# Kernel optimization log

Measured on AMD Instinct MI355X. Metric: run time of the kernel, lower is better.

Reference implementation:

```python
import jax, jax.numpy as jnp
import numpy as np

GAMMA = 0.01
INFER_STEP = 5


def softor(x, axis, gamma=GAMMA):
    # gamma * logsumexp(x / gamma) along `axis`, rescaled by global max if it exceeds 1
    y = gamma * jax.nn.logsumexp(x / gamma, axis=axis)
    mx = jnp.max(y)
    return jnp.where(mx > 1.0, y / mx, y)


def setup_inputs() -> dict:
    key = jax.random.key(0)
    k1, k2, k3 = jax.random.split(key, 3)
    B, G, C, S, L, m = 32, 2048, 16, 8, 3, 16
    x = jax.random.uniform(k1, (B, G), dtype=jnp.float32)          # valuation vector in [0,1]
    W = jax.random.normal(k2, (m, C), dtype=jnp.float32)           # clause-assignment weights
    I = jax.random.randint(k3, (C, G, S, L), 0, G)                 # index tensor into atom axis
    return {"x": x, "W": W, "I": I}


def reference(x, W, I):
    # x: [B,G] valuations; W: [m,C]; I: [C,G,S,L] int indices into G
    def r(V):
        # all C clause functions at once: gather V along atom axis using I
        gathered = V[:, I]                      # [B,C,G,S,L]
        body = jnp.prod(gathered, axis=-1)      # conjunction over body literals -> [B,C,G,S]
        Cv = softor(body, axis=-1)              # softor over substitutions -> [B,C,G]
        Ws = jax.nn.softmax(W, axis=1)          # [m,C]
        H = jnp.einsum('mc,bcg->mbg', Ws, Cv)   # weighted clause mix -> [m,B,G]
        return softor(H, axis=0)                # softor over m heads -> [B,G]

    R = x
    for _ in range(INFER_STEP):
        R = softor(jnp.stack([R, r(R)], axis=1), axis=1)  # amalgamate old and new facts
    return R
```

## Files before the change

kernel.cpp:

```cpp
#include <hip/hip_runtime.h>

#define GAMMA 0.01f
#define B 32
#define G 2048
#define C 16
#define S 8
#define L 3
#define M 16
#define NBLK 256
#define NTHR 512
#define SLOT_STRIDE 16

#define K_EXP 144.26950408889634f
#define K_LOG 0.006931471805599453f

#define SCOPE __HIP_MEMORY_SCOPE_AGENT

__device__ __forceinline__ void ast(unsigned* p, unsigned v) {
    __hip_atomic_store(p, v, __ATOMIC_RELAXED, SCOPE);
}
__device__ __forceinline__ float aldf(const float* p) {
    return __hip_atomic_load(p, __ATOMIC_RELAXED, SCOPE);
}
__device__ __forceinline__ void astf(float* p, float v) {
    __hip_atomic_store(p, v, __ATOMIC_RELAXED, SCOPE);
}

__device__ __forceinline__ float waveMax(float v) {
#pragma unroll
    for (int off = 32; off > 0; off >>= 1)
        v = fmaxf(v, __shfl_xor(v, off, 64));
    return v;
}

__device__ __forceinline__ float red8(const float* s) {
    return fmaxf(fmaxf(fmaxf(s[0], s[1]), fmaxf(s[2], s[3])),
                 fmaxf(fmaxf(s[4], s[5]), fmaxf(s[6], s[7])));
}

__device__ __forceinline__ float gridMaxBarrier(unsigned long long* slot,
                                                unsigned ep, float v,
                                                float* scratch) {
    asm volatile("s_waitcnt vmcnt(0) lgkmcnt(0)" ::: "memory");
    float wm = waveMax(v);
    __syncthreads();
    if ((threadIdx.x & 63) == 0) scratch[threadIdx.x >> 6] = wm;
    __syncthreads();
    if (threadIdx.x == 0) {
        float bm = red8(scratch);
        unsigned long long pkt = ((unsigned long long)ep << 32) |
                                 (unsigned long long)__float_as_uint(bm);
        __hip_atomic_store(&slot[(size_t)blockIdx.x * SLOT_STRIDE], pkt,
                           __ATOMIC_RELAXED, SCOPE);
    }
    unsigned long long got;
    int guard = 0;
    do {
        got = __hip_atomic_load(
            &slot[(size_t)(threadIdx.x & 255) * SLOT_STRIDE],
            __ATOMIC_RELAXED, SCOPE);
    } while ((unsigned)(got >> 32) < ep && ++guard < (1 << 17));
    float pv = waveMax(__uint_as_float((unsigned)got));
    __syncthreads();
    if ((threadIdx.x & 63) == 0) scratch[threadIdx.x >> 6] = pv;
    __syncthreads();
    return red8(scratch);
}

extern "C" __global__ __launch_bounds__(512, 2) void kmain(
    const float* __restrict__ x, const float* __restrict__ W,
    const int* __restrict__ I,
    unsigned long long* __restrict__ slotA, unsigned long long* __restrict__ slotB,
    unsigned long long* __restrict__ slotC, unsigned* __restrict__ Ipk,
    float* __restrict__ Ry, float* __restrict__ out)
{
    __shared__ __align__(16) float Vrow[G];
    __shared__ float WsL[C * M];
    __shared__ float ph[256 * 33];
    __shared__ float scratch[8];

    const int t = threadIdx.x;
    const int bid = blockIdx.x;
    const int b = bid & 31;
    const int gt = bid >> 5;
    const int ch = t >> 8;
    const int gl = t & 255;
    const int g = (gt << 8) + gl;

    if (t < 256) {
        const int m = t >> 4, c = t & 15;
        float rmax = -INFINITY;
#pragma unroll
        for (int j = 0; j < C; j++) rmax = fmaxf(rmax, W[m * C + j]);
        float rsum = 0.f;
#pragma unroll
        for (int j = 0; j < C; j++) rsum += __expf(W[m * C + j] - rmax);
        WsL[c * M + m] = __expf(W[m * C + c] - rmax) / rsum;
    }
    {
        const int tid = bid * NTHR + t;
        if (tid < C * G) {
            const int4* ip4 = (const int4*)(I + (size_t)tid * 24);
            int idx[24];
#pragma unroll
            for (int j = 0; j < 6; j++) {
                int4 v = ip4[j];
                idx[4 * j + 0] = v.x; idx[4 * j + 1] = v.y;
                idx[4 * j + 2] = v.z; idx[4 * j + 3] = v.w;
            }
            unsigned* dst = Ipk + (size_t)tid * 12;
#pragma unroll
            for (int j = 0; j < 12; j++)
                ast(&dst[j],
                    ((unsigned)idx[2 * j] << 2) | ((unsigned)idx[2 * j + 1] << 18));
        }
    }
    float m3 = gridMaxBarrier(slotC, 1, -INFINITY, scratch);

    float ry = 0.f;
    for (int it = 0; it < 5; it++) {
        float s = 1.0f;
        if (it > 0)
            s = (m3 > 1.0f) ? 1.0f / m3 : 1.0f;
        if (it == 0) {
            const float4* V4 = (const float4*)(x + (size_t)b * G);
            ((float4*)Vrow)[t] = V4[t];
        } else {
            const float* src = Ry + (size_t)b * G;
#pragma unroll
            for (int j = 0; j < 4; j++) {
                const int gg = t + j * 512;
                Vrow[gg] = s * aldf(&src[gg]);
            }
        }
        __syncthreads();

        float h[M];
#pragma unroll
        for (int m = 0; m < M; m++) h[m] = 0.f;
        float ymax = -INFINITY;
        const char* vb = (const char*)Vrow;

#pragma unroll 2
        for (int cc = 0; cc < 8; cc++) {
            const int c = ch * 8 + cc;
            const uint4* ip = (const uint4*)(Ipk + ((size_t)c * G + g) * 12);
            uint4 u0 = ip[0], u1 = ip[1], u2 = ip[2];
            unsigned w[12] = {u0.x, u0.y, u0.z, u0.w, u1.x, u1.y,
                              u1.z, u1.w, u2.x, u2.y, u2.z, u2.w};
            float vv[24];
#pragma unroll
            for (int q = 0; q < 12; q++) {
                vv[2 * q]     = *(const float*)(vb + (w[q] & 0xffffu));
                vv[2 * q + 1] = *(const float*)(vb + (w[q] >> 16));
            }
            float body[S];
#pragma unroll
            for (int ss = 0; ss < S; ss++)
                body[ss] = vv[ss * 3] * vv[ss * 3 + 1] * vv[ss * 3 + 2];
            float bm = body[0];
#pragma unroll
            for (int ss = 1; ss < S; ss++) bm = fmaxf(bm, body[ss]);
            float sum = 0.f;
#pragma unroll
            for (int ss = 0; ss < S; ss++)
                sum += exp2f((body[ss] - bm) * K_EXP);
            float y = fmaf(K_LOG, log2f(sum), bm);
            ymax = fmaxf(ymax, y);
#pragma unroll
            for (int m = 0; m < M; m++)
                h[m] = fmaf(WsL[c * M + m], y, h[m]);
        }
#pragma unroll
        for (int m = 0; m < M; m++)
            ph[gl * 33 + ch * 16 + m] = h[m];
        float m1 = gridMaxBarrier(slotA, it + 1, ymax, scratch);

        float hy = -INFINITY;
        if (t < 256) {
            float s1 = (m1 > 1.0f) ? 1.0f / m1 : 1.0f;
            float hv[M];
            float hm = -INFINITY;
#pragma unroll
            for (int m = 0; m < M; m++) {
                float hh = ph[t * 33 + m] + ph[t * 33 + 16 + m];
                hv[m] = s1 * hh;
                hm = fmaxf(hm, hv[m]);
            }
            float sum = 0.f;
#pragma unroll
            for (int m = 0; m < M; m++) sum += exp2f((hv[m] - hm) * K_EXP);
            hy = fmaf(K_LOG, log2f(sum), hm);
        }
        float m2 = gridMaxBarrier(slotB, it + 1, hy, scratch);

        float rt = -INFINITY;
        if (t < 256) {
            float s2 = (m2 > 1.0f) ? 1.0f / m2 : 1.0f;
            float Rv = Vrow[(gt << 8) + t];
            float rv = s2 * hy;
            float a = fmaxf(Rv, rv), d = fminf(Rv, rv);
            ry = fmaf(K_LOG, log2f(1.0f + exp2f((d - a) * K_EXP)), a);
            astf(&Ry[(size_t)b * G + (gt << 8) + t], ry);
            rt = ry;
        }
        m3 = gridMaxBarrier(slotC, it + 2, rt, scratch);
    }

    if (t < 256) {
        float sf = (m3 > 1.0f) ? 1.0f / m3 : 1.0f;
        out[(size_t)b * G + (gt << 8) + t] = sf * ry;
    }
}

extern "C" void kernel_launch(void* const* d_in, const int* in_sizes, int n_in,
                              void* d_out, int out_size, void* d_ws, size_t ws_size,
                              hipStream_t stream) {
    const float* x = (const float*)d_in[0];
    const float* W = (const float*)d_in[1];
    const int*   I = (const int*)d_in[2];
    float* out = (float*)d_out;

    unsigned long long* slotA = (unsigned long long*)d_ws;
    unsigned long long* slotB = slotA + NBLK * SLOT_STRIDE;
    unsigned long long* slotC = slotB + NBLK * SLOT_STRIDE;
    float* Ry = (float*)(slotC + NBLK * SLOT_STRIDE);
    unsigned* Ipk = (unsigned*)(Ry + (size_t)B * G);

    hipMemsetAsync(slotA, 0, 3 * NBLK * SLOT_STRIDE * sizeof(unsigned long long),
                   stream);

    kmain<<<dim3(NBLK), dim3(NTHR), 0, stream>>>(
        x, W, I, slotA, slotB, slotC, Ipk, Ry, out);
}
```

Baseline: 160.4 us.

## Replace flat grid max-barrier with two-level hierarchical barrier and overlap LDS reads

The grid-wide max barrier changes from every thread of every block polling all 256 per-block slots to a two-level scheme. One leader block per group of 16 reduces its group's slots and publishes the result to a group slot, and every block polls only the 16 group slots with a single wave. Per-block slots are now packed contiguously instead of strided. Some LDS reads (partial h sums, Vrow values) are moved between the arrive and wait phases so they overlap the barrier latency, and the W weights are read as float4 vectors. The extra level adds one hop of latency per barrier, and the packed slots may share cache lines.

Result: faster. 146.0 us (-9.0%).

```diff
diff --git a/kernel.cpp b/kernel.cpp
--- a/kernel.cpp
+++ b/kernel.cpp
@@ -9,7 +9,7 @@
 #define M 16
 #define NBLK 256
 #define NTHR 512
-#define SLOT_STRIDE 16
+#define GSTR 16
 
 #define K_EXP 144.26950408889634f
 #define K_LOG 0.006931471805599453f
@@ -23,6 +23,12 @@
     return __hip_atomic_load(p, __ATOMIC_RELAXED, SCOPE);
 }
 __device__ __forceinline__ void astf(float* p, float v) {
+    __hip_atomic_store(p, v, __ATOMIC_RELAXED, SCOPE);
+}
+__device__ __forceinline__ unsigned long long ald64(const unsigned long long* p) {
+    return __hip_atomic_load(p, __ATOMIC_RELAXED, SCOPE);
+}
+__device__ __forceinline__ void ast64(unsigned long long* p, unsigned long long v) {
     __hip_atomic_store(p, v, __ATOMIC_RELAXED, SCOPE);
 }
 
@@ -38,9 +44,8 @@
                  fmaxf(fmaxf(s[4], s[5]), fmaxf(s[6], s[7])));
 }
 
-__device__ __forceinline__ float gridMaxBarrier(unsigned long long* slot,
-                                                unsigned ep, float v,
-                                                float* scratch) {
+__device__ __forceinline__ void barArrive(unsigned long long* slot, unsigned ep,
+                                          float v, float* scratch) {
     asm volatile("s_waitcnt vmcnt(0) lgkmcnt(0)" ::: "memory");
     float wm = waveMax(v);
     __syncthreads();
@@ -48,34 +53,56 @@
     __syncthreads();
     if (threadIdx.x == 0) {
         float bm = red8(scratch);
-        unsigned long long pkt = ((unsigned long long)ep << 32) |
-                                 (unsigned long long)__float_as_uint(bm);
-        __hip_atomic_store(&slot[(size_t)blockIdx.x * SLOT_STRIDE], pkt,
-                           __ATOMIC_RELAXED, SCOPE);
-    }
-    unsigned long long got;
-    int guard = 0;
-    do {
-        got = __hip_atomic_load(
-            &slot[(size_t)(threadIdx.x & 255) * SLOT_STRIDE],
-            __ATOMIC_RELAXED, SCOPE);
-    } while ((unsigned)(got >> 32) < ep && ++guard < (1 << 17));
-    float pv = waveMax(__uint_as_float((unsigned)got));
+        ast64(&slot[blockIdx.x], ((unsigned long long)ep << 32) |
+                                 (unsigned long long)__float_as_uint(bm));
+    }
+}
+
+__device__ __forceinline__ float barWait(const unsigned long long* slot,
+                                         unsigned long long* gslot,
+                                         unsigned ep, float* scratch) {
+    const int t = threadIdx.x;
+    if (t < 64) {
+        if ((blockIdx.x & 15) == 0) {
+            float pv = -INFINITY;
+            if (t < 16) {
+                unsigned long long got;
+                int guard = 0;
+                do { got = ald64(&slot[blockIdx.x + t]); }
+                while ((unsigned)(got >> 32) < ep && ++guard < (1 << 17));
+                pv = __uint_as_float((unsigned)got);
+            }
+            float gm = waveMax(pv);
+            if (t == 0)
+                ast64(&gslot[(size_t)(blockIdx.x >> 4) * GSTR],
+                      ((unsigned long long)ep << 32) |
+                      (unsigned long long)__float_as_uint(gm));
+        }
+        float qv = -INFINITY;
+        if (t < 16) {
+            unsigned long long got;
+            int guard = 0;
+            do { got = ald64(&gslot[(size_t)t * GSTR]); }
+            while ((unsigned)(got >> 32) < ep && ++guard < (1 << 17));
+            qv = __uint_as_float((unsigned)got);
+        }
+        float fm = waveMax(qv);
+        if (t == 0) scratch[0] = fm;
+    }
     __syncthreads();
-    if ((threadIdx.x & 63) == 0) scratch[threadIdx.x >> 6] = pv;
-    __syncthreads();
-    return red8(scratch);
+    return scratch[0];
 }
 
 extern "C" __global__ __launch_bounds__(512, 2) void kmain(
     const float* __restrict__ x, const float* __restrict__ W,
     const int* __restrict__ I,
     unsigned long long* __restrict__ slotA, unsigned long long* __restrict__ slotB,
-    unsigned long long* __restrict__ slotC, unsigned* __restrict__ Ipk,
-    float* __restrict__ Ry, float* __restrict__ out)
+    unsigned long long* __restrict__ slotC, unsigned long long* __restrict__ gslotA,
+    unsigned long long* __restrict__ gslotB, unsigned long long* __restrict__ gslotC,
+    unsigned* __restrict__ Ipk, float* __restrict__ Ry, float* __restrict__ out)
 {
     __shared__ __align__(16) float Vrow[G];
-    __shared__ float WsL[C * M];
+    __shared__ __align__(16) float WsL[C * M];
     __shared__ float ph[256 * 33];
     __shared__ float scratch[8];
 
@@ -115,7 +142,8 @@
                     ((unsigned)idx[2 * j] << 2) | ((unsigned)idx[2 * j + 1] << 18));
         }
     }
-    float m3 = gridMaxBarrier(slotC, 1, -INFINITY, scratch);
+    barArrive(slotC, 1, -INFINITY, scratch);
+    float m3 = barWait(slotC, gslotC, 1, scratch);
 
     float ry = 0.f;
     for (int it = 0; it < 5; it++) {
@@ -167,14 +195,25 @@
                 sum += exp2f((body[ss] - bm) * K_EXP);
             float y = fmaf(K_LOG, log2f(sum), bm);
             ymax = fmaxf(ymax, y);
+            const float4* Wc = (const float4*)&WsL[c * M];
+            float4 w0 = Wc[0], w1 = Wc[1], w2 = Wc[2], w3 = Wc[3];
+            const float wv[16] = {w0.x, w0.y, w0.z, w0.w, w1.x, w1.y, w1.z, w1.w,
+                                  w2.x, w2.y, w2.z, w2.w, w3.x, w3.y, w3.z, w3.w};
 #pragma unroll
             for (int m = 0; m < M; m++)
-                h[m] = fmaf(WsL[c * M + m], y, h[m]);
+                h[m] = fmaf(wv[m], y, h[m]);
         }
 #pragma unroll
         for (int m = 0; m < M; m++)
             ph[gl * 33 + ch * 16 + m] = h[m];
-        float m1 = gridMaxBarrier(slotA, it + 1, ymax, scratch);
+        barArrive(slotA, it + 1, ymax, scratch);
+        float hraw[M];
+        if (t < 256) {
+#pragma unroll
+            for (int m = 0; m < M; m++)
+                hraw[m] = ph[t * 33 + m] + ph[t * 33 + 16 + m];
+        }
+        float m1 = barWait(slotA, gslotA, it + 1, scratch);
 
         float hy = -INFINITY;
         if (t < 256) {
@@ -183,8 +222,7 @@
             float hm = -INFINITY;
 #pragma unroll
             for (int m = 0; m < M; m++) {
-                float hh = ph[t * 33 + m] + ph[t * 33 + 16 + m];
-                hv[m] = s1 * hh;
+                hv[m] = s1 * hraw[m];
                 hm = fmaxf(hm, hv[m]);
             }
             float sum = 0.f;
@@ -192,19 +230,21 @@
             for (int m = 0; m < M; m++) sum += exp2f((hv[m] - hm) * K_EXP);
             hy = fmaf(K_LOG, log2f(sum), hm);
         }
-        float m2 = gridMaxBarrier(slotB, it + 1, hy, scratch);
+        barArrive(slotB, it + 1, hy, scratch);
+        float Rv = (t < 256) ? Vrow[(gt << 8) + t] : 0.f;
+        float m2 = barWait(slotB, gslotB, it + 1, scratch);
 
         float rt = -INFINITY;
         if (t < 256) {
             float s2 = (m2 > 1.0f) ? 1.0f / m2 : 1.0f;
-            float Rv = Vrow[(gt << 8) + t];
             float rv = s2 * hy;
             float a = fmaxf(Rv, rv), d = fminf(Rv, rv);
             ry = fmaf(K_LOG, log2f(1.0f + exp2f((d - a) * K_EXP)), a);
             astf(&Ry[(size_t)b * G + (gt << 8) + t], ry);
             rt = ry;
         }
-        m3 = gridMaxBarrier(slotC, it + 2, rt, scratch);
+        barArrive(slotC, it + 2, rt, scratch);
+        m3 = barWait(slotC, gslotC, it + 2, scratch);
     }
 
     if (t < 256) {
@@ -221,15 +261,18 @@
     const int*   I = (const int*)d_in[2];
     float* out = (float*)d_out;
 
-    unsigned long long* slotA = (unsigned long long*)d_ws;
-    unsigned long long* slotB = slotA + NBLK * SLOT_STRIDE;
-    unsigned long long* slotC = slotB + NBLK * SLOT_STRIDE;
-    float* Ry = (float*)(slotC + NBLK * SLOT_STRIDE);
+    unsigned long long* slotA  = (unsigned long long*)d_ws;
+    unsigned long long* slotB  = slotA + NBLK;
+    unsigned long long* slotC  = slotB + NBLK;
+    unsigned long long* gslotA = slotC + NBLK;
+    unsigned long long* gslotB = gslotA + 16 * GSTR;
+    unsigned long long* gslotC = gslotB + 16 * GSTR;
+    float* Ry = (float*)(gslotC + 16 * GSTR);
     unsigned* Ipk = (unsigned*)(Ry + (size_t)B * G);
 
-    hipMemsetAsync(slotA, 0, 3 * NBLK * SLOT_STRIDE * sizeof(unsigned long long),
+    hipMemsetAsync(slotA, 0, (3 * NBLK + 3 * 16 * GSTR) * sizeof(unsigned long long),
                    stream);
 
     kmain<<<dim3(NBLK), dim3(NTHR), 0, stream>>>(
-        x, W, I, slotA, slotB, slotC, Ipk, Ry, out);
-}
+        x, W, I, slotA, slotB, slotC, gslotA, gslotB, gslotC, Ipk, Ry, out);
+}
```
